# Performance work log

Hardware: AMD Instinct MI355X
Metric: run time of the kernel (lower is better)

## Reference

```python
import jax, jax.numpy as jnp
import numpy as np

N_NODES = 50000
N_RELS = 50
N_CLASSES = 40
EMB_DIM = 16
RP = 16
N_TRIPLES = 400000


def setup_inputs() -> dict:
    rng = np.random.default_rng(0)
    s = rng.integers(0, N_NODES, size=N_TRIPLES)
    r = rng.integers(0, N_RELS, size=N_TRIPLES)
    o = rng.integers(0, N_NODES, size=N_TRIPLES)
    # unique (s,o) pairs, as in torch.unique(pairs, dim=0, return_inverse=True)
    pairs = np.stack([s, o], axis=1)
    unique_pairs, inverse = np.unique(pairs, axis=0, return_inverse=True)
    nt = unique_pairs.shape[0]
    # relation_matrix COO (nt, num_rels), coalesced (duplicate (row,col) summed)
    keys = inverse.astype(np.int64) * N_RELS + r
    uk, counts = np.unique(keys, return_counts=True)
    rm_rows = (uk // N_RELS).astype(np.int32)
    rm_cols = (uk % N_RELS).astype(np.int32)
    rm_vals = counts.astype(np.float32)
    # hindices / vindices exactly as in __init__ (note o*rm / s*rm construction)
    s_u = unique_pairs[:, 0].astype(np.int64)
    o_u = unique_pairs[:, 1].astype(np.int64)
    rm = np.arange(RP, dtype=np.int64)[:, None]            # (rp, 1)
    h_rows = np.broadcast_to(s_u[None, :], (RP, nt)).reshape(-1).astype(np.int32)
    h_cols = (o_u[None, :] * rm).reshape(-1).astype(np.int32)
    v_rows = (s_u[None, :] * rm).reshape(-1).astype(np.int32)
    v_cols = np.broadcast_to(o_u[None, :], (RP, nt)).reshape(-1).astype(np.int32)
    # float params (xavier-like scale for weights, randn for rel emb, zero biases)
    key = jax.random.key(0)
    k1, k2, k3 = jax.random.split(key, 3)
    gain = np.sqrt(2.0)  # relu gain
    w1_std = gain * np.sqrt(2.0 / (N_NODES + EMB_DIM))
    w2_std = gain * np.sqrt(2.0 / (EMB_DIM + N_CLASSES))
    return {
        'rel_emb': jax.random.normal(k1, (N_RELS, RP), dtype=jnp.float32),
        'weights1': jax.random.normal(k2, (RP, N_NODES, EMB_DIM), dtype=jnp.float32) * w1_std,
        'weights2': jax.random.normal(k3, (RP, EMB_DIM, N_CLASSES), dtype=jnp.float32) * w2_std,
        'bias1': jnp.zeros((EMB_DIM,), dtype=jnp.float32),
        'bias2': jnp.zeros((N_CLASSES,), dtype=jnp.float32),
        'rm_rows': jnp.asarray(rm_rows),
        'rm_cols': jnp.asarray(rm_cols),
        'rm_vals': jnp.asarray(rm_vals),
        'h_rows': jnp.asarray(h_rows),
        'h_cols': jnp.asarray(h_cols),
        'v_rows': jnp.asarray(v_rows),
        'v_cols': jnp.asarray(v_cols),
    }


def reference(rel_emb, weights1, weights2, bias1, bias2,
              rm_rows, rm_cols, rm_vals, h_rows, h_cols, v_rows, v_cols):
    rp, n, e = weights1.shape
    nt = h_rows.shape[0] // rp
    # latents = sparse.mm(relation_matrix, relation_embeddings) -> (nt, rp)
    latents = jax.ops.segment_sum(rm_vals[:, None] * rel_emb[rm_cols], rm_rows,
                                  num_segments=nt)
    latents = jax.nn.softmax(latents, axis=1)
    lf = latents.T.reshape(-1)                              # (rp*nt,)
    # sum_sparse(hindices, lf, (n, n*rp), row=False): per-column sums, gathered
    colsum = jax.ops.segment_sum(lf, h_cols, num_segments=n * rp)
    ln = lf / colsum[h_cols]
    # spmm(hindices, ln, (n, n*rp), weights1_flat) -> (n, e)
    w1f = weights1.reshape(rp * n, e)
    h = jax.ops.segment_sum(ln[:, None] * w1f[h_cols], h_rows, num_segments=n)
    h = jax.nn.relu(h + bias1)
    # sum_sparse(vindices, lf, (n*rp, n), row=True): per-row sums, gathered
    rowsum = jax.ops.segment_sum(lf, v_rows, num_segments=n * rp)
    ln2 = lf / rowsum[v_rows]
    # spmm(vindices, ln2, (n*rp, n), h) -> (n*rp, e)
    h2 = jax.ops.segment_sum(ln2[:, None] * h[v_cols], v_rows, num_segments=n * rp)
    h2 = h2.reshape(rp, n, e)
    out = jnp.einsum('rhc,rnh->nc', weights2, h2) + bias2
    return out
```

## Files before the change

kernel.cpp:

```cpp
#include <hip/hip_runtime.h>

#define RP 16
#define EMB 16
#define NC 40

#define BCASTF(dst, srci, R) \
    dst = __int_as_float(__builtin_amdgcn_mov_dpp(srci, 0x150 + R, 0xf, 0xf, true));

__global__ void k_count(const int* __restrict__ s_u, const int* __restrict__ o_u,
                        int* __restrict__ cnt_s, int* __restrict__ cnt_o, int nt) {
    int t = blockIdx.x * blockDim.x + threadIdx.x;
    if (t < nt) {
        atomicAdd(&cnt_s[s_u[t]], 1);
        atomicAdd(&cnt_o[o_u[t]], 1);
    }
}

__global__ void k_scan_blk(const int* __restrict__ cnt_s, int* __restrict__ offs_s,
                           const int* __restrict__ cnt_o, int* __restrict__ offs_o,
                           int* __restrict__ partials, int n, int nblk) {
    const int* in = blockIdx.y ? cnt_o : cnt_s;
    int* out = blockIdx.y ? offs_o : offs_s;
    int tid = threadIdx.x;
    int i0 = blockIdx.x * 1024 + tid * 4;
    int v[4];
    #pragma unroll
    for (int q = 0; q < 4; ++q) {
        int i = i0 + q;
        v[q] = (i < n) ? in[i] : 0;
    }
    int tsum = v[0] + v[1] + v[2] + v[3];
    int lane = tid & 63, wid = tid >> 6;
    int x = tsum;
    #pragma unroll
    for (int d = 1; d < 64; d <<= 1) {
        int u = __shfl_up(x, d, 64);
        if (lane >= d) x += u;
    }
    __shared__ int wsum[4];
    if (lane == 63) wsum[wid] = x;
    __syncthreads();
    int woff = 0;
    for (int wq = 0; wq < wid; ++wq) woff += wsum[wq];
    int run = woff + x - tsum;
    #pragma unroll
    for (int q = 0; q < 4; ++q) {
        int i = i0 + q;
        if (i < n) out[i] = run;
        run += v[q];
    }
    if (tid == 255) partials[blockIdx.y * nblk + blockIdx.x] = run;
}

__global__ void k_scan_top(int* __restrict__ partials, int nblk) {
    int w = threadIdx.x >> 6;
    int lane = threadIdx.x & 63;
    int carry = 0;
    for (int base = 0; base < nblk; base += 64) {
        int idx = base + lane;
        int v = (idx < nblk) ? partials[w * nblk + idx] : 0;
        int x = v;
        #pragma unroll
        for (int d = 1; d < 64; d <<= 1) {
            int u = __shfl_up(x, d, 64);
            if (lane >= d) x += u;
        }
        if (idx < nblk) partials[w * nblk + idx] = carry + x - v;
        carry += __shfl(x, 63, 64);
    }
}

__global__ void k_scan_add(int* __restrict__ offs_s, int* __restrict__ cur_s,
                           int* __restrict__ offs_o, int* __restrict__ cur_o,
                           const int* __restrict__ partials, int n, int nblk) {
    int* out = blockIdx.y ? offs_o : offs_s;
    int* cur = blockIdx.y ? cur_o : cur_s;
    int add = partials[blockIdx.y * nblk + blockIdx.x];
    int i0 = blockIdx.x * 1024 + threadIdx.x * 4;
    #pragma unroll
    for (int q = 0; q < 4; ++q) {
        int i = i0 + q;
        if (i < n) {
            int vv = out[i] + add;
            out[i] = vv;
            cur[i] = vv;
        }
    }
}

__global__ void k_latents(const float* __restrict__ rel_emb,
                          const int* __restrict__ rows,
                          const int* __restrict__ cols,
                          const float* __restrict__ vals,
                          const int* __restrict__ s_u,
                          const int* __restrict__ o_u,
                          int* __restrict__ cur_o,
                          float* __restrict__ lat_t, float* __restrict__ lat_o,
                          float* __restrict__ lat0, int* __restrict__ su_o,
                          int nm) {
    int i = blockIdx.x * blockDim.x + threadIdx.x;
    int e = i >> 4, k = i & 15;
    if (e >= nm) return;
    int row = rows[e];
    if (e > 0 && rows[e - 1] == row) return;
    float acc = vals[e] * rel_emb[cols[e] * RP + k];
    while (e + 1 < nm && rows[e + 1] == row) {
        ++e;
        acc += vals[e] * rel_emb[cols[e] * RP + k];
    }
    float m = acc;
    #pragma unroll
    for (int d = 1; d < 16; d <<= 1) m = fmaxf(m, __shfl_xor(m, d, 16));
    float v = expf(acc - m);
    float s = v;
    #pragma unroll
    for (int d = 1; d < 16; d <<= 1) s += __shfl_xor(s, d, 16);
    v = v / s;
    lat_t[(size_t)row * RP + k] = v;
    int po = 0;
    if (k == 0) {
        int ou = o_u[row];
        po = atomicAdd(&cur_o[ou], 1);
        su_o[po] = s_u[row];
        lat0[row] = v;
    }
    po = __shfl(po, 0, 16);
    lat_o[(size_t)po * RP + k] = v;
}

__global__ void k_r0(const float* __restrict__ lat0,
                     float* __restrict__ rowsum, float* __restrict__ colsum,
                     int nt) {
    float acc = 0.f;
    for (int t = blockIdx.x * blockDim.x + threadIdx.x; t < nt;
         t += gridDim.x * blockDim.x)
        acc += lat0[t];
    #pragma unroll
    for (int d = 32; d; d >>= 1) acc += __shfl_down(acc, d, 64);
    __shared__ float sm[4];
    int lane = threadIdx.x & 63, wid = threadIdx.x >> 6;
    if (lane == 0) sm[wid] = acc;
    __syncthreads();
    if (threadIdx.x == 0) {
        float tot = sm[0] + sm[1] + sm[2] + sm[3];
        atomicAdd(&rowsum[0], tot);
        atomicAdd(&colsum[0], tot);
    }
}

__global__ void k_latsum(const float* __restrict__ lat_o,
                         const int* __restrict__ offs_o,
                         const int* __restrict__ cnt_o,
                         float* __restrict__ colsum, int n) {
    int i = blockIdx.x * blockDim.x + threadIdx.x;
    int v = i >> 4, k = i & 15;
    if (v >= n) return;
    int beg = offs_o[v], d = cnt_o[v];
    if (d == 0) return;
    float ls = 0.f;
    int j = 0;
    for (; j + 4 <= d; j += 4) {
        float a0 = lat_o[(size_t)(beg + j + 0) * RP + k];
        float a1 = lat_o[(size_t)(beg + j + 1) * RP + k];
        float a2 = lat_o[(size_t)(beg + j + 2) * RP + k];
        float a3 = lat_o[(size_t)(beg + j + 3) * RP + k];
        ls += (a0 + a1) + (a2 + a3);
    }
    for (; j < d; ++j) ls += lat_o[(size_t)(beg + j) * RP + k];
    if (k >= 1) atomicAdd(&colsum[(size_t)v * k], ls);
}

__global__ void k_h_acc(const float* __restrict__ lat_o,
                        const int* __restrict__ offs_o,
                        const int* __restrict__ cnt_o,
                        const int* __restrict__ su_o,
                        const float* __restrict__ colsum,
                        const float* __restrict__ w1,
                        float* __restrict__ h, int n) {
    int i = blockIdx.x * blockDim.x + threadIdx.x;
    int o = i >> 4, k = i & 15;
    if (o >= n) return;
    int d = cnt_o[o];
    if (d == 0) return;
    int beg = offs_o[o];
    float W[RP];
    #pragma unroll
    for (int r = 0; r < RP; ++r)
        W[r] = w1[(size_t)(o * r) * EMB + k];
    float rcp_cs = 1.f / colsum[(size_t)o * k];
    for (int j0 = 0; j0 < d; j0 += 16) {
        int su16 = su_o[beg + min(j0 + k, d - 1)];
        float la[16];
        #pragma unroll
        for (int e = 0; e < 16; ++e)
            la[e] = lat_o[(size_t)(beg + min(j0 + e, d - 1)) * RP + k];
        #pragma unroll
        for (int e = 0; e < 16; ++e) {
            if (j0 + e >= d) break;
            float ln = la[e] * rcp_cs;
            int ln_i = __float_as_int(ln);
            float acc = 0.f, b;
            #define HACC_STEP(R) BCASTF(b, ln_i, R); acc = fmaf(b, W[R], acc);
            HACC_STEP(0)  HACC_STEP(1)  HACC_STEP(2)  HACC_STEP(3)
            HACC_STEP(4)  HACC_STEP(5)  HACC_STEP(6)  HACC_STEP(7)
            HACC_STEP(8)  HACC_STEP(9)  HACC_STEP(10) HACC_STEP(11)
            HACC_STEP(12) HACC_STEP(13) HACC_STEP(14) HACC_STEP(15)
            #undef HACC_STEP
            int s = __shfl(su16, e, 16);
            atomicAdd(&h[s * EMB + k], acc);
        }
    }
}

__global__ void k_h2(const float* __restrict__ lat_t,
                     const int* __restrict__ offs_s,
                     const int* __restrict__ cnt_s,
                     const int* __restrict__ o_u,
                     float* __restrict__ rowsum,
                     const float* __restrict__ h,
                     const float* __restrict__ bias1,
                     float* __restrict__ h2,
                     float* __restrict__ r0part, int n) {
    __shared__ float r0acc[EMB];
    if (threadIdx.x < EMB) r0acc[threadIdx.x] = 0.f;
    __syncthreads();
    int i = blockIdx.x * blockDim.x + threadIdx.x;
    int s = i >> 4, k = i & 15;
    float b1k = bias1[k];
    float M[RP];
    #pragma unroll
    for (int r = 0; r < RP; ++r) M[r] = 0.f;
    float rs_acc = 0.f;
    int d = 0;
    if (s < n) {
        int beg = offs_s[s];
        d = cnt_s[s];
        for (int j0 = 0; j0 < d; j0 += 16) {
            int o16 = o_u[beg + min(j0 + k, d - 1)];
            float hv[16], la[16];
            #pragma unroll
            for (int e = 0; e < 16; ++e) {
                int oe = __shfl(o16, e, 16);
                hv[e] = h[(size_t)oe * EMB + k];
                la[e] = lat_t[(size_t)(beg + min(j0 + e, d - 1)) * RP + k];
            }
            #pragma unroll
            for (int e = 0; e < 16; ++e) {
                if (j0 + e >= d) break;
                float hvr = fmaxf(hv[e] + b1k, 0.f);
                rs_acc += la[e];
                int lat_i = __float_as_int(la[e]);
                float b;
                #define H2_STEP(R) BCASTF(b, lat_i, R); M[R] = fmaf(b, hvr, M[R]);
                H2_STEP(0)  H2_STEP(1)  H2_STEP(2)  H2_STEP(3)
                H2_STEP(4)  H2_STEP(5)  H2_STEP(6)  H2_STEP(7)
                H2_STEP(8)  H2_STEP(9)  H2_STEP(10) H2_STEP(11)
                H2_STEP(12) H2_STEP(13) H2_STEP(14) H2_STEP(15)
                #undef H2_STEP
            }
        }
    }
    if (s < n && d > 0) {
        if (k >= 1) atomicAdd(&rowsum[(size_t)s * k], rs_acc);
        atomicAdd(&r0acc[k], M[0]);
        #pragma unroll
        for (int r = 1; r < RP; ++r)
            atomicAdd(&h2[(size_t)(s * r) * EMB + k], M[r]);
    }
    __syncthreads();
    if (threadIdx.x < EMB)
        r0part[(size_t)blockIdx.x * EMB + threadIdx.x] = r0acc[threadIdx.x];
}

__global__ void k_h2r0(const float* __restrict__ r0part,
                       float* __restrict__ h2, int nblk) {
    __shared__ float red[1024];
    int k = threadIdx.x & 15, j0 = threadIdx.x >> 4;
    float acc = 0.f;
    for (int j = j0; j < nblk; j += 64)
        acc += r0part[(size_t)j * EMB + k];
    red[j0 * 16 + k] = acc;
    __syncthreads();
    #pragma unroll
    for (int st = 32; st >= 1; st >>= 1) {
        if (j0 < st) red[j0 * 16 + k] += red[(j0 + st) * 16 + k];
        __syncthreads();
    }
    if (threadIdx.x < 16) h2[threadIdx.x] += red[threadIdx.x];
}

#define CB2 20
__global__ void k_out(const float* __restrict__ w2,
                      const float* __restrict__ bias2,
                      const float* __restrict__ h2,
                      const float* __restrict__ rowsum,
                      float* __restrict__ out, int n) {
    __shared__ float w2s[RP * EMB * NC];
    for (int i = threadIdx.x; i < RP * EMB * NC; i += 256)
        w2s[i] = w2[i];
    __syncthreads();
    int gi = blockIdx.x * blockDim.x + threadIdx.x;
    int node = gi >> 1;
    int c0 = (gi & 1) * CB2;
    if (node >= n) return;
    float acc[CB2];
    #pragma unroll
    for (int c = 0; c < CB2; ++c) acc[c] = bias2[c0 + c];
    for (int rq = 0; rq < RP; ++rq) {
        size_t flat = (size_t)rq * n + node;
        float rs = rowsum[flat];
        float rcp = (rs != 0.f) ? 1.f / rs : 0.f;
        const float4* h2row = (const float4*)&h2[flat * EMB];
        float4 hv4[4];
        #pragma unroll
        for (int q = 0; q < 4; ++q) hv4[q] = h2row[q];
        const float* hv = (const float*)hv4;
        #pragma unroll
        for (int hh = 0; hh < EMB; ++hh) {
            const float4* wrow = (const float4*)&w2s[(rq * EMB + hh) * NC + c0];
            float hvv = hv[hh] * rcp;
            #pragma unroll
            for (int q5 = 0; q5 < 5; ++q5) {
                float4 wv = wrow[q5];
                acc[q5 * 4 + 0] += wv.x * hvv;
                acc[q5 * 4 + 1] += wv.y * hvv;
                acc[q5 * 4 + 2] += wv.z * hvv;
                acc[q5 * 4 + 3] += wv.w * hvv;
            }
        }
    }
    float4* op = (float4*)&out[node * NC + c0];
    #pragma unroll
    for (int q5 = 0; q5 < 5; ++q5)
        op[q5] = make_float4(acc[q5 * 4], acc[q5 * 4 + 1],
                             acc[q5 * 4 + 2], acc[q5 * 4 + 3]);
}

extern "C" void kernel_launch(void* const* d_in, const int* in_sizes, int n_in,
                              void* d_out, int out_size, void* d_ws, size_t ws_size,
                              hipStream_t stream) {
    const float* rel_emb = (const float*)d_in[0];
    const float* w1      = (const float*)d_in[1];
    const float* w2      = (const float*)d_in[2];
    const float* b1      = (const float*)d_in[3];
    const float* b2      = (const float*)d_in[4];
    const int*   rm_rows = (const int*)d_in[5];
    const int*   rm_cols = (const int*)d_in[6];
    const float* rm_vals = (const float*)d_in[7];
    const int*   h_rows  = (const int*)d_in[8];
    const int*   v_cols  = (const int*)d_in[11];

    const int nm = in_sizes[5];
    const int ne = in_sizes[8];
    const int nt = ne / RP;
    const int n  = in_sizes[1] / (RP * EMB);

    const int B = 256;
    const int nblk_h2 = (n * 16 + B - 1) / B;
    const int nblk_sc = (n + 1023) / 1024;

    char* w = (char*)d_ws;
    float* colsum = (float*)w;  w += (size_t)n * RP * 4;
    float* rowsum = (float*)w;  w += (size_t)n * RP * 4;
    float* h2     = (float*)w;  w += (size_t)n * RP * EMB * 4;
    float* h      = (float*)w;  w += (size_t)n * EMB * 4;
    int* cnt_s    = (int*)w;    w += (size_t)n * 4;
    int* cnt_o    = (int*)w;    w += (size_t)n * 4;
    size_t zero_bytes = (size_t)(w - (char*)d_ws);
    float* lat_t  = (float*)w;  w += (size_t)nt * RP * 4;
    float* lat_o  = (float*)w;  w += (size_t)nt * RP * 4;
    float* lat0   = (float*)w;  w += (size_t)nt * 4;
    int* su_o     = (int*)w;    w += (size_t)nt * 4;
    int* offs_s   = (int*)w;    w += (size_t)n * 4;
    int* cur_s    = (int*)w;    w += (size_t)n * 4;
    int* offs_o   = (int*)w;    w += (size_t)n * 4;
    int* cur_o    = (int*)w;    w += (size_t)n * 4;
    float* r0part = (float*)w;  w += (size_t)nblk_h2 * EMB * 4;
    int* partials = (int*)w;    w += (size_t)2 * nblk_sc * 4;
    if ((size_t)(w - (char*)d_ws) > ws_size) return;

    hipMemsetAsync(d_ws, 0, zero_bytes, stream);

    k_count<<<dim3((nt + B - 1) / B), dim3(B), 0, stream>>>(
        h_rows, v_cols, cnt_s, cnt_o, nt);
    k_scan_blk<<<dim3(nblk_sc, 2), dim3(B), 0, stream>>>(
        cnt_s, offs_s, cnt_o, offs_o, partials, n, nblk_sc);
    k_scan_top<<<dim3(1), dim3(128), 0, stream>>>(partials, nblk_sc);
    k_scan_add<<<dim3(nblk_sc, 2), dim3(B), 0, stream>>>(
        offs_s, cur_s, offs_o, cur_o, partials, n, nblk_sc);
    k_latents<<<dim3((nm * 16 + B - 1) / B), dim3(B), 0, stream>>>(
        rel_emb, rm_rows, rm_cols, rm_vals, h_rows, v_cols,
        cur_o, lat_t, lat_o, lat0, su_o, nm);
    k_r0<<<dim3(64), dim3(B), 0, stream>>>(lat0, rowsum, colsum, nt);
    k_latsum<<<dim3((n * 16 + B - 1) / B), dim3(B), 0, stream>>>(
        lat_o, offs_o, cnt_o, colsum, n);
    k_h_acc<<<dim3((n * 16 + B - 1) / B), dim3(B), 0, stream>>>(
        lat_o, offs_o, cnt_o, su_o, colsum, w1, h, n);
    k_h2<<<dim3(nblk_h2), dim3(B), 0, stream>>>(
        lat_t, offs_s, cnt_s, v_cols, rowsum, h, b1, h2, r0part, n);
    k_h2r0<<<dim3(1), dim3(1024), 0, stream>>>(r0part, h2, nblk_h2);
    k_out<<<dim3((n * 2 + B - 1) / B), dim3(B), 0, stream>>>(
        w2, b2, h2, rowsum, (float*)d_out, n);
}
```

Before: 270.3 us.

## Replace scattered h2 atomics with per-source M2 writes gathered in output kernel

k_h2 now stores its 15 per-relation partial results into a dense per-source buffer M2 with plain stores, replacing atomicAdds into the scattered h2 rows s*r. k_out rebuilds each h2 row by testing divisibility of the flat index by every r and gathering the matching M2 rows, with row 0 taken from the reduced g0. This removes global atomics and the memset of the large h2 buffer. In exchange k_out does integer divisions and scattered reads over up to 15 candidate rows.

```diff
diff --git a/kernel.cpp b/kernel.cpp
--- a/kernel.cpp
+++ b/kernel.cpp
@@ -219,7 +219,7 @@
                      float* __restrict__ rowsum,
                      const float* __restrict__ h,
                      const float* __restrict__ bias1,
-                     float* __restrict__ h2,
+                     float* __restrict__ M2,
                      float* __restrict__ r0part, int n) {
     __shared__ float r0acc[EMB];
     if (threadIdx.x < EMB) r0acc[threadIdx.x] = 0.f;
@@ -260,12 +260,15 @@
             }
         }
     }
-    if (s < n && d > 0) {
-        if (k >= 1) atomicAdd(&rowsum[(size_t)s * k], rs_acc);
-        atomicAdd(&r0acc[k], M[0]);
+    if (s < n) {
+        if (d > 0) {
+            if (k >= 1) atomicAdd(&rowsum[(size_t)s * k], rs_acc);
+            atomicAdd(&r0acc[k], M[0]);
+        }
+        float* dst = &M2[(size_t)s * 15 * EMB + k];
         #pragma unroll
         for (int r = 1; r < RP; ++r)
-            atomicAdd(&h2[(size_t)(s * r) * EMB + k], M[r]);
+            dst[(size_t)(r - 1) * EMB] = M[r];
     }
     __syncthreads();
     if (threadIdx.x < EMB)
@@ -273,7 +276,7 @@
 }
 
 __global__ void k_h2r0(const float* __restrict__ r0part,
-                       float* __restrict__ h2, int nblk) {
+                       float* __restrict__ g0, int nblk) {
     __shared__ float red[1024];
     int k = threadIdx.x & 15, j0 = threadIdx.x >> 4;
     float acc = 0.f;
@@ -286,13 +289,14 @@
         if (j0 < st) red[j0 * 16 + k] += red[(j0 + st) * 16 + k];
         __syncthreads();
     }
-    if (threadIdx.x < 16) h2[threadIdx.x] += red[threadIdx.x];
+    if (threadIdx.x < 16) g0[threadIdx.x] = red[threadIdx.x];
 }
 
 #define CB2 20
 __global__ void k_out(const float* __restrict__ w2,
                       const float* __restrict__ bias2,
-                      const float* __restrict__ h2,
+                      const float* __restrict__ M2,
+                      const float* __restrict__ g0,
                       const float* __restrict__ rowsum,
                       float* __restrict__ out, int n) {
     __shared__ float w2s[RP * EMB * NC];
@@ -307,14 +311,34 @@
     #pragma unroll
     for (int c = 0; c < CB2; ++c) acc[c] = bias2[c0 + c];
     for (int rq = 0; rq < RP; ++rq) {
-        size_t flat = (size_t)rq * n + node;
-        float rs = rowsum[flat];
+        int m = rq * n + node;
+        float rs = rowsum[m];
         float rcp = (rs != 0.f) ? 1.f / rs : 0.f;
-        const float4* h2row = (const float4*)&h2[flat * EMB];
-        float4 hv4[4];
-        #pragma unroll
-        for (int q = 0; q < 4; ++q) hv4[q] = h2row[q];
-        const float* hv = (const float*)hv4;
+        float hv[EMB];
+        #pragma unroll
+        for (int q = 0; q < EMB; ++q) hv[q] = 0.f;
+        if (m == 0) {
+            #pragma unroll
+            for (int q = 0; q < EMB; ++q) hv[q] = g0[q];
+        }
+        #pragma unroll
+        for (int r = 1; r < RP; ++r) {
+            if (m % r == 0) {
+                int s = m / r;
+                if (s < n) {
+                    const float4* row =
+                        (const float4*)&M2[((size_t)s * 15 + (r - 1)) * EMB];
+                    #pragma unroll
+                    for (int q = 0; q < 4; ++q) {
+                        float4 v = row[q];
+                        hv[q * 4 + 0] += v.x;
+                        hv[q * 4 + 1] += v.y;
+                        hv[q * 4 + 2] += v.z;
+                        hv[q * 4 + 3] += v.w;
+                    }
+                }
+            }
+        }
         #pragma unroll
         for (int hh = 0; hh < EMB; ++hh) {
             const float4* wrow = (const float4*)&w2s[(rq * EMB + hh) * NC + c0];
@@ -362,11 +386,11 @@
     char* w = (char*)d_ws;
     float* colsum = (float*)w;  w += (size_t)n * RP * 4;
     float* rowsum = (float*)w;  w += (size_t)n * RP * 4;
-    float* h2     = (float*)w;  w += (size_t)n * RP * EMB * 4;
     float* h      = (float*)w;  w += (size_t)n * EMB * 4;
     int* cnt_s    = (int*)w;    w += (size_t)n * 4;
     int* cnt_o    = (int*)w;    w += (size_t)n * 4;
     size_t zero_bytes = (size_t)(w - (char*)d_ws);
+    float* M2     = (float*)w;  w += (size_t)n * 15 * EMB * 4;
     float* lat_t  = (float*)w;  w += (size_t)nt * RP * 4;
     float* lat_o  = (float*)w;  w += (size_t)nt * RP * 4;
     float* lat0   = (float*)w;  w += (size_t)nt * 4;
@@ -376,6 +400,7 @@
     int* offs_o   = (int*)w;    w += (size_t)n * 4;
     int* cur_o    = (int*)w;    w += (size_t)n * 4;
     float* r0part = (float*)w;  w += (size_t)nblk_h2 * EMB * 4;
+    float* g0     = (float*)w;  w += (size_t)EMB * 4;
     int* partials = (int*)w;    w += (size_t)2 * nblk_sc * 4;
     if ((size_t)(w - (char*)d_ws) > ws_size) return;
 
@@ -397,8 +422,8 @@
     k_h_acc<<<dim3((n * 16 + B - 1) / B), dim3(B), 0, stream>>>(
         lat_o, offs_o, cnt_o, su_o, colsum, w1, h, n);
     k_h2<<<dim3(nblk_h2), dim3(B), 0, stream>>>(
-        lat_t, offs_s, cnt_s, v_cols, rowsum, h, b1, h2, r0part, n);
-    k_h2r0<<<dim3(1), dim3(1024), 0, stream>>>(r0part, h2, nblk_h2);
+        lat_t, offs_s, cnt_s, v_cols, rowsum, h, b1, M2, r0part, n);
+    k_h2r0<<<dim3(1), dim3(1024), 0, stream>>>(r0part, g0, nblk_h2);
     k_out<<<dim3((n * 2 + B - 1) / B), dim3(B), 0, stream>>>(
-        w2, b2, h2, rowsum, (float*)d_out, n);
-}
+        w2, b2, M2, g0, rowsum, (float*)d_out, n);
+}
```

New measurement: 271.9 us. No clear change (+0.6%).
